# Performance work log

Hardware: AMD Instinct MI355X
Metric: run time of the kernel (lower is better)

The kernel has to match this reference:

```python
import jax, jax.numpy as jnp
import numpy as np

C = 128   # in_channels == global_graph_width (required by residual add)
W = 128
LN_EPS = 1e-5


def _mlp3(x, Ws, bs):
    # three stacked Linear layers (Dense dropout is identity in eval)
    for i in range(3):
        x = x @ Ws[i].T + bs[i]
    return x


def setup_inputs() -> dict:
    key = jax.random.key(0)
    ks = jax.random.split(key, 12)
    B, N, M = 16, 2048, 2048
    x1 = jax.random.normal(ks[0], (B, N, C), dtype=jnp.float32)
    x2 = jax.random.normal(ks[1], (B, M, C), dtype=jnp.float32)
    valid_mask = jax.random.randint(ks[2], (B, N, M), 0, 2) == 1
    s = 1.0 / np.sqrt(C)
    q_w = jax.random.normal(ks[3], (3, W, C), dtype=jnp.float32) * s
    q_b = jnp.zeros((3, W), dtype=jnp.float32)
    k_w = jax.random.normal(ks[4], (3, W, C), dtype=jnp.float32) * s
    k_b = jnp.zeros((3, W), dtype=jnp.float32)
    v_w = jax.random.normal(ks[5], (3, W, C), dtype=jnp.float32) * s
    v_b = jnp.zeros((3, W), dtype=jnp.float32)
    ln_g = jnp.ones((W,), dtype=jnp.float32)
    ln_b = jnp.zeros((W,), dtype=jnp.float32)
    return {"x1": x1, "x2": x2, "valid_mask": valid_mask,
            "q_w": q_w, "q_b": q_b, "k_w": k_w, "k_b": k_b,
            "v_w": v_w, "v_b": v_b, "ln_g": ln_g, "ln_b": ln_b}


def reference(x1, x2, valid_mask, q_w, q_b, k_w, k_b, v_w, v_b, ln_g, ln_b):
    query = _mlp3(x1, q_w, q_b)          # [B,N,W]
    key = _mlp3(x2, k_w, k_b)            # [B,M,W]
    value = _mlp3(x2, v_w, v_b)          # [B,M,W]
    scores = jnp.einsum('bnw,bmw->bnm', query, key) / jnp.sqrt(jnp.float32(W))
    # masked softmax: masked_fill(True -> -1e12), softmax, then zero masked cols
    scores = jnp.where(valid_mask, jnp.float32(-1e12), scores)
    attn = jax.nn.softmax(scores, axis=-1) * (1.0 - valid_mask.astype(scores.dtype))
    x = jnp.einsum('bnm,bmw->bnw', attn, value)  # [B,N,W]
    mu = jnp.mean(x, axis=-1, keepdims=True)
    var = jnp.var(x, axis=-1, keepdims=True)
    ln = (x - mu) / jnp.sqrt(var + LN_EPS) * ln_g + ln_b
    return ln + x1
```

## Files before the change

kernel.cpp:

```cpp
#include <hip/hip_runtime.h>
#include <hip/hip_bf16.h>
#include <hip/hip_fp16.h>

typedef __hip_bfloat16 bf16;
typedef __attribute__((ext_vector_type(8))) short short8;
typedef __attribute__((ext_vector_type(4))) float f32x4;

#define MFMA(a, b, c) __builtin_amdgcn_mfma_f32_16x16x32_bf16((a), (b), (c), 0, 0, 0)
#define SPLIT 2

__global__ void detect_mask(const unsigned int* __restrict__ m, int* __restrict__ flag)
{
    __shared__ int bad;
    if (threadIdx.x == 0) bad = 0;
    __syncthreads();
    unsigned int w = m[threadIdx.x];
    bool ok = (w == 0u) || (w == 1u) || (w == 0x3F800000u);
    if (!ok) atomicAdd(&bad, 1);
    __syncthreads();
    if (threadIdx.x == 0) *flag = (bad == 0) ? 0 : 1;
}

__global__ void compose_a(const float* __restrict__ qw, const float* __restrict__ qb,
                          const float* __restrict__ kw, const float* __restrict__ kb,
                          const float* __restrict__ vw, const float* __restrict__ vb,
                          float* __restrict__ T, float* __restrict__ bt)
{
    int h = blockIdx.x >> 7;
    int i = blockIdx.x & 127;
    int j = threadIdx.x;
    const float* W = (h == 0) ? qw : (h == 1) ? kw : vw;
    const float* bv = (h == 0) ? qb : (h == 1) ? kb : vb;
    const float* W1 = W;
    const float* W2 = W + 128 * 128;
    float acc = 0.f;
    for (int k = 0; k < 128; ++k) acc += W2[i * 128 + k] * W1[k * 128 + j];
    T[h * 16384 + i * 128 + j] = acc;
    if (j == 0) {
        float bacc = 0.f;
        for (int k = 0; k < 128; ++k) bacc += W2[i * 128 + k] * bv[k];
        bt[h * 128 + i] = bacc + bv[128 + i];
    }
}

__global__ void compose_b(const float* __restrict__ qw, const float* __restrict__ qb,
                          const float* __restrict__ kw, const float* __restrict__ kb,
                          const float* __restrict__ vw, const float* __restrict__ vb,
                          const float* __restrict__ T, const float* __restrict__ bt,
                          bf16* __restrict__ Weff, float* __restrict__ beff)
{
    int h = blockIdx.x >> 7;
    int i = blockIdx.x & 127;
    int j = threadIdx.x;
    const float* W = (h == 0) ? qw : (h == 1) ? kw : vw;
    const float* bv = (h == 0) ? qb : (h == 1) ? kb : vb;
    const float* W3 = W + 2 * 128 * 128;
    const float* Th = T + h * 16384;
    float acc = 0.f;
    for (int k = 0; k < 128; ++k) acc += W3[i * 128 + k] * Th[k * 128 + j];
    float scale = (h == 0) ? (1.4426950408889634f * rsqrtf(128.0f)) : 1.0f;
    Weff[h * 16384 + i * 128 + j] = __float2bfloat16(acc * scale);
    if (j == 0) {
        float bacc = 0.f;
        for (int k = 0; k < 128; ++k) bacc += W3[i * 128 + k] * bt[h * 128 + k];
        beff[h * 128 + i] = (bacc + bv[256 + i]) * scale;
    }
}

__global__ __launch_bounds__(256) void proj_rm(
    const float* __restrict__ X, const bf16* __restrict__ Wb,
    const float* __restrict__ bias, bf16* __restrict__ Y)
{
    __shared__ alignas(16) char sX[64 * 256];
    int tid = threadIdx.x;
    int lane = tid & 63, wave = tid >> 6;
    int l16 = lane & 15, lhi = lane >> 4;
    long long r0 = (long long)blockIdx.x * 64;
    {
        int row = tid >> 2, seg = tid & 3;
        const float4* src = reinterpret_cast<const float4*>(X + (r0 + row) * 128 + seg * 32);
        int swz = (row & 7) << 4;
        char* dst0 = &sX[0] + row * 256;
#pragma unroll
        for (int i = 0; i < 8; ++i) {
            float4 v = src[i];
            bf16* d = (bf16*)(dst0 + ((seg * 64 + i * 8) ^ swz));
            d[0] = __float2bfloat16(v.x); d[1] = __float2bfloat16(v.y);
            d[2] = __float2bfloat16(v.z); d[3] = __float2bfloat16(v.w);
        }
    }
    __syncthreads();
    int rloc = wave * 16 + l16;
    int swzr = (rloc & 7) << 4;
    short8 a[4];
#pragma unroll
    for (int c4 = 0; c4 < 4; ++c4)
        a[c4] = *(const short8*)(&sX[0] + ((rloc * 256 + lhi * 16 + c4 * 64) ^ swzr));
    f32x4 acc[8] = {};
#pragma unroll
    for (int n = 0; n < 8; ++n) {
        const bf16* wr = Wb + (n * 16 + l16) * 128 + lhi * 8;
#pragma unroll
        for (int c4 = 0; c4 < 4; ++c4)
            acc[n] = MFMA(a[c4], *(const short8*)(wr + c4 * 32), acc[n]);
    }
#pragma unroll
    for (int n = 0; n < 8; ++n) {
        float bia = bias[l16 + 16 * n];
#pragma unroll
        for (int r = 0; r < 4; ++r) {
            long long q = r0 + wave * 16 + lhi * 4 + r;
            Y[q * 128 + l16 + 16 * n] = __float2bfloat16(acc[n][r] + bia);
        }
    }
}

__global__ __launch_bounds__(256) void proj_kf(
    const float* __restrict__ X, const bf16* __restrict__ Wb,
    const float* __restrict__ bias, bf16* __restrict__ Kf)
{
    __shared__ alignas(16) char sX[64 * 256];
    int tid = threadIdx.x;
    int lane = tid & 63, wave = tid >> 6;
    int l16 = lane & 15, lhi = lane >> 4;
    long long r0 = (long long)blockIdx.x * 64;
    {
        int row = tid >> 2, seg = tid & 3;
        const float4* src = reinterpret_cast<const float4*>(X + (r0 + row) * 128 + seg * 32);
        int swz = (row & 7) << 4;
        char* dst0 = &sX[0] + row * 256;
#pragma unroll
        for (int i = 0; i < 8; ++i) {
            float4 v = src[i];
            bf16* d = (bf16*)(dst0 + ((seg * 64 + i * 8) ^ swz));
            d[0] = __float2bfloat16(v.x); d[1] = __float2bfloat16(v.y);
            d[2] = __float2bfloat16(v.z); d[3] = __float2bfloat16(v.w);
        }
    }
    __syncthreads();
    int rloc = wave * 16 + l16;
    int swzr = (rloc & 7) << 4;
    short8 a[4];
#pragma unroll
    for (int c4 = 0; c4 < 4; ++c4)
        a[c4] = *(const short8*)(&sX[0] + ((rloc * 256 + lhi * 16 + c4 * 64) ^ swzr));
    f32x4 acc[8] = {};
#pragma unroll
    for (int n = 0; n < 8; ++n) {
        const bf16* wr = Wb + (n * 16 + l16) * 128 + lhi * 8;
#pragma unroll
        for (int c4 = 0; c4 < 4; ++c4)
            acc[n] = MFMA(a[c4], *(const short8*)(wr + c4 * 32), acc[n]);
    }
    __syncthreads();
#pragma unroll
    for (int n = 0; n < 8; ++n) {
        float bia = bias[l16 + 16 * n];
#pragma unroll
        for (int r = 0; r < 4; ++r) {
            int row = wave * 16 + lhi * 4 + r;
            *(bf16*)(&sX[0] + ((row * 256 + (l16 + 16 * n) * 2) ^ ((row & 7) << 4))) =
                __float2bfloat16(acc[n][r] + bia);
        }
    }
    __syncthreads();
#pragma unroll
    for (int c4 = 0; c4 < 4; ++c4) {
        int row = wave * 16 + l16;
        short8 v = *(const short8*)(&sX[0] +
            ((row * 256 + c4 * 64 + lhi * 16) ^ ((row & 7) << 4)));
        long long tile = (r0 >> 4) + wave;
        *(short8*)(Kf + (tile * 4 + c4) * 512 + lane * 8) = v;
    }
}

__global__ __launch_bounds__(256) void proj_vf(
    const float* __restrict__ X2, const bf16* __restrict__ Wv,
    const float* __restrict__ bias, bf16* __restrict__ Vf, int M)
{
    __shared__ alignas(16) char sX[64 * 256];
    int tid = threadIdx.x;
    int lane = tid & 63, wave = tid >> 6;
    int l16 = lane & 15, lhi = lane >> 4;
    int mtiles = M >> 6;
    int b = blockIdx.x / mtiles, mt = blockIdx.x % mtiles;
    int m0 = mt * 64;
    {
        int row = tid >> 2, seg = tid & 3;
        const float4* src = reinterpret_cast<const float4*>(
            X2 + ((long long)b * M + m0 + row) * 128 + seg * 32);
        int swz = (row & 7) << 4;
        char* dst0 = &sX[0] + row * 256;
#pragma unroll
        for (int i = 0; i < 8; ++i) {
            float4 v = src[i];
            bf16* d = (bf16*)(dst0 + ((seg * 64 + i * 8) ^ swz));
            d[0] = __float2bfloat16(v.x); d[1] = __float2bfloat16(v.y);
            d[2] = __float2bfloat16(v.z); d[3] = __float2bfloat16(v.w);
        }
    }
    __syncthreads();
    int w0 = wave * 32;
    short8 a[2][4];
#pragma unroll
    for (int wt = 0; wt < 2; ++wt) {
        const bf16* wr = Wv + (w0 + wt * 16 + l16) * 128 + lhi * 8;
#pragma unroll
        for (int c4 = 0; c4 < 4; ++c4) a[wt][c4] = *(const short8*)(wr + c4 * 32);
    }
    f32x4 acc[2][4] = {};
#pragma unroll
    for (int mtl = 0; mtl < 4; ++mtl) {
        int rloc = mtl * 16 + l16;
        int swzr = (rloc & 7) << 4;
#pragma unroll
        for (int c4 = 0; c4 < 4; ++c4) {
            short8 xb = *(const short8*)(&sX[0] + ((rloc * 256 + lhi * 16 + c4 * 64) ^ swzr));
            acc[0][mtl] = MFMA(a[0][c4], xb, acc[0][mtl]);
            acc[1][mtl] = MFMA(a[1][c4], xb, acc[1][mtl]);
        }
    }
    __syncthreads();
#pragma unroll
    for (int wt = 0; wt < 2; ++wt) {
#pragma unroll
        for (int r = 0; r < 4; ++r) {
            int w = w0 + wt * 16 + lhi * 4 + r;
            float bia = bias[w];
#pragma unroll
            for (int mtl = 0; mtl < 4; ++mtl) {
                int mloc = mtl * 16 + l16;
                *(bf16*)(&sX[0] + ((w * 128 + mloc * 2) ^ ((w & 7) << 4))) =
                    __float2bfloat16(acc[wt][mtl][r] + bia);
            }
        }
    }
    __syncthreads();
#pragma unroll
    for (int q = 0; q < 4; ++q) {
        int fr = wave * 4 + q;
        int gloc = fr >> 3, n = fr & 7;
        int row = n * 16 + l16;
        short8 v = *(const short8*)(&sX[0] +
            ((row * 128 + gloc * 64 + lhi * 16) ^ ((row & 7) << 4)));
        long long g = (long long)b * (M >> 5) + (m0 >> 5) + gloc;
        *(short8*)(Vf + (g * 8 + n) * 512 + lane * 8) = v;
    }
}

__global__ __launch_bounds__(256, 4) void attn_split(
    const bf16* __restrict__ Q, const bf16* __restrict__ Kf, const bf16* __restrict__ Vf,
    const void* __restrict__ maskp, const int* __restrict__ flagp,
    __half* __restrict__ pacc, float* __restrict__ pml,
    int B, int N, int M)
{
    __shared__ alignas(16) char kbuf[2][8192];
    __shared__ alignas(16) char vbuf[2][8192];
    __shared__ alignas(16) char Plds[4][1024];
    __shared__ alignas(16) unsigned char smask[4][512];
    int nq = N >> 6;
    int nwg = gridDim.x;
    int bid = blockIdx.x;
    int wg = ((nwg & 7) == 0) ? ((bid & 7) * (nwg >> 3) + (bid >> 3)) : bid;
    int qt = wg % nq;
    int s  = (wg / nq) % SPLIT;
    int b  = wg / (nq * SPLIT);
    int tid = threadIdx.x;
    int lane = tid & 63, wave = tid >> 6;
    int l16 = lane & 15, lhi = lane >> 4;
    int q0 = qt * 64 + wave * 16;
    int Mh = M / SPLIT;
    int mbase = s * Mh;
    long long R = (long long)B * N;
    int fl4 = (*flagp == 0);
    const int NT = Mh >> 5;

    const bf16* qptr = Q + ((long long)b * N + q0 + l16) * 128 + lhi * 8;
    short8 aq[4];
#pragma unroll
    for (int c4 = 0; c4 < 4; ++c4) aq[c4] = *(const short8*)(qptr + c4 * 32);

    long long ktile0 = ((long long)b * M + mbase) >> 4;
    long long gbase  = ((long long)b * M + mbase) >> 5;

    int srow = lane >> 2, soff = (lane & 3) * 8;
    long long mrowb = ((long long)b * N + q0 + srow) * (long long)M + mbase + soff;

    char* pb = &Plds[wave][0];
    unsigned char* smw = &smask[wave][0];
    int pswz = (l16 & 3) << 4;

    f32x4 acc[8] = {};
    float plsum = 0.f;

    auto mload = [&](int t) -> uint2 {
        uint2 r;
        if (fl4) {
            const int* mp = (const int*)maskp;
            const int4* pp = (const int4*)(mp + mrowb + (long long)t * 32);
            int4 a = pp[0], bb = pp[1];
            r.x = (a.x ? 1u : 0u) | ((a.y ? 1u : 0u) << 8) |
                  ((a.z ? 1u : 0u) << 16) | ((a.w ? 1u : 0u) << 24);
            r.y = (bb.x ? 1u : 0u) | ((bb.y ? 1u : 0u) << 8) |
                  ((bb.z ? 1u : 0u) << 16) | ((bb.w ? 1u : 0u) << 24);
        } else {
            r = *(const uint2*)((const unsigned char*)maskp + mrowb + (long long)t * 32);
        }
        return r;
    };

    {
        long long F = ktile0 * 4 + wave * 2;
        long long G = gbase * 8 + wave * 2;
        int4 k0 = *(const int4*)(Kf + F * 512 + lane * 8);
        int4 k1 = *(const int4*)(Kf + (F + 1) * 512 + lane * 8);
        int4 v0 = *(const int4*)(Vf + G * 512 + lane * 8);
        int4 v1 = *(const int4*)(Vf + (G + 1) * 512 + lane * 8);
        uint2 mreg = mload(0);
        *(int4*)(&kbuf[0][(wave * 2 + 0) * 1024 + lane * 16]) = k0;
        *(int4*)(&kbuf[0][(wave * 2 + 1) * 1024 + lane * 16]) = k1;
        *(int4*)(&vbuf[0][(wave * 2 + 0) * 1024 + lane * 16]) = v0;
        *(int4*)(&vbuf[0][(wave * 2 + 1) * 1024 + lane * 16]) = v1;
        *(uint2*)(smw + srow * 32 + soff) = mreg;
        __syncthreads();
    }

    for (int t = 0; t < NT; ++t) {
        int cur = t & 1;
        int4 ks0, ks1, vs0, vs1;
        uint2 mreg;
        bool nxt = (t + 1 < NT);
        if (nxt) {
            long long F = (ktile0 + 2LL * (t + 1)) * 4 + wave * 2;
            long long G = (gbase + (t + 1)) * 8 + wave * 2;
            ks0 = *(const int4*)(Kf + F * 512 + lane * 8);
            ks1 = *(const int4*)(Kf + (F + 1) * 512 + lane * 8);
            vs0 = *(const int4*)(Vf + G * 512 + lane * 8);
            vs1 = *(const int4*)(Vf + (G + 1) * 512 + lane * 8);
            mreg = mload(t + 1);
        }

        f32x4 sv[2];
#pragma unroll
        for (int j = 0; j < 2; ++j) {
            f32x4 tt = {0.f, 0.f, 0.f, 0.f};
#pragma unroll
            for (int c4 = 0; c4 < 4; ++c4)
                tt = MFMA(*(const short8*)(&kbuf[cur][(j * 4 + c4) * 1024 + lane * 16]),
                          aq[c4], tt);
            sv[j] = tt;
        }

#pragma unroll
        for (int j = 0; j < 2; ++j) {
            unsigned int mk = *(const unsigned int*)(smw + l16 * 32 + 16 * j + lhi * 4);
            float p0 = (mk & 0x000000ffu) ? 0.f : exp2f(sv[j][0]);
            float p1 = (mk & 0x0000ff00u) ? 0.f : exp2f(sv[j][1]);
            float p2 = (mk & 0x00ff0000u) ? 0.f : exp2f(sv[j][2]);
            float p3 = (mk & 0xff000000u) ? 0.f : exp2f(sv[j][3]);
            plsum += (p0 + p1) + (p2 + p3);
            unsigned int w0, w1;
            asm("v_cvt_pk_bf16_f32 %0, %1, %2" : "=v"(w0) : "v"(p0), "v"(p1));
            asm("v_cvt_pk_bf16_f32 %0, %1, %2" : "=v"(w1) : "v"(p2), "v"(p3));
            uint2 wv; wv.x = w0; wv.y = w1;
            *(uint2*)(pb + l16 * 64 + ((j * 32 + lhi * 8) ^ pswz)) = wv;
        }

        short8 pa = *(const short8*)(pb + l16 * 64 + ((lhi * 16) ^ pswz));

#pragma unroll
        for (int n = 0; n < 8; ++n)
            acc[n] = MFMA(pa, *(const short8*)(&vbuf[cur][n * 1024 + lane * 16]), acc[n]);

        if (nxt) {
            int nx = cur ^ 1;
            *(int4*)(&kbuf[nx][(wave * 2 + 0) * 1024 + lane * 16]) = ks0;
            *(int4*)(&kbuf[nx][(wave * 2 + 1) * 1024 + lane * 16]) = ks1;
            *(int4*)(&vbuf[nx][(wave * 2 + 0) * 1024 + lane * 16]) = vs0;
            *(int4*)(&vbuf[nx][(wave * 2 + 1) * 1024 + lane * 16]) = vs1;
            *(uint2*)(smw + srow * 32 + soff) = mreg;
            __syncthreads();
        }
    }

    float lsum = plsum;
    lsum += __shfl_xor(lsum, 16);
    lsum += __shfl_xor(lsum, 32);
    float invq = (lsum > 0.f) ? 1.f / lsum : 0.f;
    float inv[4];
#pragma unroll
    for (int r = 0; r < 4; ++r) inv[r] = __shfl(invq, lhi * 4 + r);
    long long rowg[4];
#pragma unroll
    for (int r = 0; r < 4; ++r) rowg[r] = (long long)b * N + q0 + lhi * 4 + r;
#pragma unroll
    for (int n = 0; n < 8; ++n)
#pragma unroll
        for (int r = 0; r < 4; ++r)
            pacc[((long long)s * R + rowg[r]) * 128 + l16 + 16 * n] =
                __float2half(acc[n][r] * inv[r]);
    if (lhi == 0)
        pml[(long long)s * R + (long long)b * N + q0 + l16] = lsum;
}

__global__ __launch_bounds__(256) void combine(
    const __half* __restrict__ pacc, const float* __restrict__ pml,
    const float* __restrict__ lng, const float* __restrict__ lnb,
    const float* __restrict__ x1, float* __restrict__ out, long long R)
{
    int tid = threadIdx.x;
    int lane = tid & 63, wave = tid >> 6;
    long long row = (long long)blockIdx.x * 4 + wave;
    float l[SPLIT];
    float den = 0.f;
#pragma unroll
    for (int s = 0; s < SPLIT; ++s) {
        l[s] = pml[(long long)s * R + row];
        den += l[s];
    }
    float inv = (den > 0.f) ? 1.f / den : 0.f;
    int c0 = lane * 2;
    float xa = 0.f, xb = 0.f;
#pragma unroll
    for (int s = 0; s < SPLIT; ++s) {
        const __half* hp = pacc + ((long long)s * R + row) * 128 + c0;
        xa += l[s] * __half2float(hp[0]);
        xb += l[s] * __half2float(hp[1]);
    }
    xa *= inv; xb *= inv;
    float su = xa + xb;
#pragma unroll
    for (int o = 1; o < 64; o <<= 1) su += __shfl_xor(su, o);
    float mu = su * (1.f / 128.f);
    float da = xa - mu, db = xb - mu;
    float sq = da * da + db * db;
#pragma unroll
    for (int o = 1; o < 64; o <<= 1) sq += __shfl_xor(sq, o);
    float rstd = rsqrtf(sq * (1.f / 128.f) + 1e-5f);
    float2 xr = *(const float2*)(x1 + row * 128 + c0);
    float2 o2;
    o2.x = da * rstd * lng[c0] + lnb[c0] + xr.x;
    o2.y = db * rstd * lng[c0 + 1] + lnb[c0 + 1] + xr.y;
    *(float2*)(out + row * 128 + c0) = o2;
}

extern "C" void kernel_launch(void* const* d_in, const int* in_sizes, int n_in,
                              void* d_out, int out_size, void* d_ws, size_t ws_size,
                              hipStream_t stream)
{
    const float* x1 = (const float*)d_in[0];
    const float* x2 = (const float*)d_in[1];
    const void* mask = d_in[2];
    const float* qw = (const float*)d_in[3];
    const float* qb = (const float*)d_in[4];
    const float* kw = (const float*)d_in[5];
    const float* kb = (const float*)d_in[6];
    const float* vw = (const float*)d_in[7];
    const float* vb = (const float*)d_in[8];
    const float* lng = (const float*)d_in[9];
    const float* lnb = (const float*)d_in[10];

    long long a = (long long)in_sizes[0] / 128;
    long long c = (long long)in_sizes[1] / 128;
    long long mm = (long long)in_sizes[2];
    int B = (int)((a * c) / mm);
    int N = (int)(a / B);
    int M = (int)(c / B);
    long long R = a;

    char* p = (char*)d_ws;
    bf16* Q = (bf16*)p;    p += (size_t)a * 128 * sizeof(bf16);
    bf16* Kf = (bf16*)p;   p += (size_t)c * 128 * sizeof(bf16);
    bf16* Vf = (bf16*)p;   p += (size_t)c * 128 * sizeof(bf16);
    float* T = (float*)p;  p += 3 * 128 * 128 * sizeof(float);
    float* bt = (float*)p; p += 3 * 128 * sizeof(float);
    float* beff = (float*)p; p += 3 * 128 * sizeof(float);
    bf16* Weff = (bf16*)p; p += 3 * 128 * 128 * sizeof(bf16);
    int* flag = (int*)p;   p += 256;
    __half* pacc = (__half*)p; p += (size_t)SPLIT * R * 128 * sizeof(__half);
    float* pml = (float*)p;    p += (size_t)SPLIT * R * sizeof(float);

    detect_mask<<<1, 256, 0, stream>>>((const unsigned int*)mask, flag);
    compose_a<<<384, 128, 0, stream>>>(qw, qb, kw, kb, vw, vb, T, bt);
    compose_b<<<384, 128, 0, stream>>>(qw, qb, kw, kb, vw, vb, T, bt, Weff, beff);

    proj_rm<<<(int)(a / 64), 256, 0, stream>>>(x1, Weff, beff, Q);
    proj_kf<<<(int)(c / 64), 256, 0, stream>>>(x2, Weff + 16384, beff + 128, Kf);
    proj_vf<<<(int)(c / 64), 256, 0, stream>>>(x2, Weff + 2 * 16384, beff + 256, Vf, M);

    int nblk = B * (N / 64) * SPLIT;
    attn_split<<<nblk, 256, 0, stream>>>(Q, Kf, Vf, mask, flag, pacc, pml, B, N, M);
    combine<<<(int)(R / 4), 256, 0, stream>>>(pacc, pml, lng, lnb, x1, (float*)d_out, R);
}
```

Baseline: 165.6 us.

## Fuse K/V projections and pass P between MFMAs via lane shuffles

Merges the separate K and V projection kernels into one that loads and converts x2 to bf16 once, using a second LDS buffer for output staging. In the attention loop, the probability tile is now rearranged from the QK MFMA output layout into the PV MFMA input layout with two cross-lane shuffles instead of an LDS write and read. The per-wave P LDS buffer is removed, and the MFMA sections are wrapped in s_setprio to favour matrix issue. This saves one launch and one pass over x2, and cuts LDS traffic in the hot loop. The cost is extra shuffle and select instructions, plus more LDS in the projection kernel.

```diff
diff --git a/kernel.cpp b/kernel.cpp
--- a/kernel.cpp
+++ b/kernel.cpp
@@ -115,18 +115,23 @@
     }
 }
 
-__global__ __launch_bounds__(256) void proj_kf(
-    const float* __restrict__ X, const bf16* __restrict__ Wb,
-    const float* __restrict__ bias, bf16* __restrict__ Kf)
+__global__ __launch_bounds__(256) void proj_kvf(
+    const float* __restrict__ X2,
+    const bf16* __restrict__ Wk, const float* __restrict__ bk,
+    const bf16* __restrict__ Wv, const float* __restrict__ bv,
+    bf16* __restrict__ Kf, bf16* __restrict__ Vf, int M)
 {
     __shared__ alignas(16) char sX[64 * 256];
+    __shared__ alignas(16) char rbuf[64 * 256];
     int tid = threadIdx.x;
     int lane = tid & 63, wave = tid >> 6;
     int l16 = lane & 15, lhi = lane >> 4;
     long long r0 = (long long)blockIdx.x * 64;
+    int b = (int)(r0 / M);
+    int m0 = (int)(r0 % M);
     {
         int row = tid >> 2, seg = tid & 3;
-        const float4* src = reinterpret_cast<const float4*>(X + (r0 + row) * 128 + seg * 32);
+        const float4* src = reinterpret_cast<const float4*>(X2 + (r0 + row) * 128 + seg * 32);
         int swz = (row & 7) << 4;
         char* dst0 = &sX[0] + row * 256;
 #pragma unroll
@@ -138,77 +143,52 @@
         }
     }
     __syncthreads();
-    int rloc = wave * 16 + l16;
-    int swzr = (rloc & 7) << 4;
-    short8 a[4];
-#pragma unroll
-    for (int c4 = 0; c4 < 4; ++c4)
-        a[c4] = *(const short8*)(&sX[0] + ((rloc * 256 + lhi * 16 + c4 * 64) ^ swzr));
-    f32x4 acc[8] = {};
-#pragma unroll
-    for (int n = 0; n < 8; ++n) {
-        const bf16* wr = Wb + (n * 16 + l16) * 128 + lhi * 8;
+
+    {
+        int rloc = wave * 16 + l16;
+        int swzr = (rloc & 7) << 4;
+        short8 a[4];
 #pragma unroll
         for (int c4 = 0; c4 < 4; ++c4)
-            acc[n] = MFMA(a[c4], *(const short8*)(wr + c4 * 32), acc[n]);
-    }
-    __syncthreads();
-#pragma unroll
-    for (int n = 0; n < 8; ++n) {
-        float bia = bias[l16 + 16 * n];
-#pragma unroll
-        for (int r = 0; r < 4; ++r) {
-            int row = wave * 16 + lhi * 4 + r;
-            *(bf16*)(&sX[0] + ((row * 256 + (l16 + 16 * n) * 2) ^ ((row & 7) << 4))) =
-                __float2bfloat16(acc[n][r] + bia);
+            a[c4] = *(const short8*)(&sX[0] + ((rloc * 256 + lhi * 16 + c4 * 64) ^ swzr));
+        f32x4 acc[8] = {};
+#pragma unroll
+        for (int n = 0; n < 8; ++n) {
+            const bf16* wr = Wk + (n * 16 + l16) * 128 + lhi * 8;
+#pragma unroll
+            for (int c4 = 0; c4 < 4; ++c4)
+                acc[n] = MFMA(a[c4], *(const short8*)(wr + c4 * 32), acc[n]);
+        }
+#pragma unroll
+        for (int n = 0; n < 8; ++n) {
+            float bia = bk[l16 + 16 * n];
+#pragma unroll
+            for (int r = 0; r < 4; ++r) {
+                int row = wave * 16 + lhi * 4 + r;
+                *(bf16*)(&rbuf[0] + ((row * 256 + (l16 + 16 * n) * 2) ^ ((row & 7) << 4))) =
+                    __float2bfloat16(acc[n][r] + bia);
+            }
         }
     }
     __syncthreads();
 #pragma unroll
     for (int c4 = 0; c4 < 4; ++c4) {
         int row = wave * 16 + l16;
-        short8 v = *(const short8*)(&sX[0] +
+        short8 v = *(const short8*)(&rbuf[0] +
             ((row * 256 + c4 * 64 + lhi * 16) ^ ((row & 7) << 4)));
         long long tile = (r0 >> 4) + wave;
         *(short8*)(Kf + (tile * 4 + c4) * 512 + lane * 8) = v;
     }
-}
-
-__global__ __launch_bounds__(256) void proj_vf(
-    const float* __restrict__ X2, const bf16* __restrict__ Wv,
-    const float* __restrict__ bias, bf16* __restrict__ Vf, int M)
-{
-    __shared__ alignas(16) char sX[64 * 256];
-    int tid = threadIdx.x;
-    int lane = tid & 63, wave = tid >> 6;
-    int l16 = lane & 15, lhi = lane >> 4;
-    int mtiles = M >> 6;
-    int b = blockIdx.x / mtiles, mt = blockIdx.x % mtiles;
-    int m0 = mt * 64;
-    {
-        int row = tid >> 2, seg = tid & 3;
-        const float4* src = reinterpret_cast<const float4*>(
-            X2 + ((long long)b * M + m0 + row) * 128 + seg * 32);
-        int swz = (row & 7) << 4;
-        char* dst0 = &sX[0] + row * 256;
-#pragma unroll
-        for (int i = 0; i < 8; ++i) {
-            float4 v = src[i];
-            bf16* d = (bf16*)(dst0 + ((seg * 64 + i * 8) ^ swz));
-            d[0] = __float2bfloat16(v.x); d[1] = __float2bfloat16(v.y);
-            d[2] = __float2bfloat16(v.z); d[3] = __float2bfloat16(v.w);
-        }
-    }
-    __syncthreads();
+
     int w0 = wave * 32;
-    short8 a[2][4];
+    short8 a2[2][4];
 #pragma unroll
     for (int wt = 0; wt < 2; ++wt) {
         const bf16* wr = Wv + (w0 + wt * 16 + l16) * 128 + lhi * 8;
 #pragma unroll
-        for (int c4 = 0; c4 < 4; ++c4) a[wt][c4] = *(const short8*)(wr + c4 * 32);
-    }
-    f32x4 acc[2][4] = {};
+        for (int c4 = 0; c4 < 4; ++c4) a2[wt][c4] = *(const short8*)(wr + c4 * 32);
+    }
+    f32x4 acc2[2][4] = {};
 #pragma unroll
     for (int mtl = 0; mtl < 4; ++mtl) {
         int rloc = mtl * 16 + l16;
@@ -216,8 +196,8 @@
 #pragma unroll
         for (int c4 = 0; c4 < 4; ++c4) {
             short8 xb = *(const short8*)(&sX[0] + ((rloc * 256 + lhi * 16 + c4 * 64) ^ swzr));
-            acc[0][mtl] = MFMA(a[0][c4], xb, acc[0][mtl]);
-            acc[1][mtl] = MFMA(a[1][c4], xb, acc[1][mtl]);
+            acc2[0][mtl] = MFMA(a2[0][c4], xb, acc2[0][mtl]);
+            acc2[1][mtl] = MFMA(a2[1][c4], xb, acc2[1][mtl]);
         }
     }
     __syncthreads();
@@ -226,12 +206,12 @@
 #pragma unroll
         for (int r = 0; r < 4; ++r) {
             int w = w0 + wt * 16 + lhi * 4 + r;
-            float bia = bias[w];
+            float bia = bv[w];
 #pragma unroll
             for (int mtl = 0; mtl < 4; ++mtl) {
                 int mloc = mtl * 16 + l16;
-                *(bf16*)(&sX[0] + ((w * 128 + mloc * 2) ^ ((w & 7) << 4))) =
-                    __float2bfloat16(acc[wt][mtl][r] + bia);
+                *(bf16*)(&rbuf[0] + ((w * 128 + mloc * 2) ^ ((w & 7) << 4))) =
+                    __float2bfloat16(acc2[wt][mtl][r] + bia);
             }
         }
     }
@@ -241,7 +221,7 @@
         int fr = wave * 4 + q;
         int gloc = fr >> 3, n = fr & 7;
         int row = n * 16 + l16;
-        short8 v = *(const short8*)(&sX[0] +
+        short8 v = *(const short8*)(&rbuf[0] +
             ((row * 128 + gloc * 64 + lhi * 16) ^ ((row & 7) << 4)));
         long long g = (long long)b * (M >> 5) + (m0 >> 5) + gloc;
         *(short8*)(Vf + (g * 8 + n) * 512 + lane * 8) = v;
@@ -256,7 +236,6 @@
 {
     __shared__ alignas(16) char kbuf[2][8192];
     __shared__ alignas(16) char vbuf[2][8192];
-    __shared__ alignas(16) char Plds[4][1024];
     __shared__ alignas(16) unsigned char smask[4][512];
     int nq = N >> 6;
     int nwg = gridDim.x;
@@ -286,9 +265,7 @@
     int srow = lane >> 2, soff = (lane & 3) * 8;
     long long mrowb = ((long long)b * N + q0 + srow) * (long long)M + mbase + soff;
 
-    char* pb = &Plds[wave][0];
     unsigned char* smw = &smask[wave][0];
-    int pswz = (l16 & 3) << 4;
 
     f32x4 acc[8] = {};
     float plsum = 0.f;
@@ -340,6 +317,7 @@
             mreg = mload(t + 1);
         }
 
+        __builtin_amdgcn_s_setprio(1);
         f32x4 sv[2];
 #pragma unroll
         for (int j = 0; j < 2; ++j) {
@@ -350,7 +328,9 @@
                           aq[c4], tt);
             sv[j] = tt;
         }
-
+        __builtin_amdgcn_s_setprio(0);
+
+        uint2 Bb[2];
 #pragma unroll
         for (int j = 0; j < 2; ++j) {
             unsigned int mk = *(const unsigned int*)(smw + l16 * 32 + 16 * j + lhi * 4);
@@ -362,15 +342,28 @@
             unsigned int w0, w1;
             asm("v_cvt_pk_bf16_f32 %0, %1, %2" : "=v"(w0) : "v"(p0), "v"(p1));
             asm("v_cvt_pk_bf16_f32 %0, %1, %2" : "=v"(w1) : "v"(p2), "v"(p3));
-            uint2 wv; wv.x = w0; wv.y = w1;
-            *(uint2*)(pb + l16 * 64 + ((j * 32 + lhi * 8) ^ pswz)) = wv;
-        }
-
-        short8 pa = *(const short8*)(pb + l16 * 64 + ((lhi * 16) ^ pswz));
-
+            Bb[j].x = w0; Bb[j].y = w1;
+        }
+
+        uint2 X1 = (lhi < 2) ? Bb[1] : Bb[0];
+        uint2 Qb;
+        Qb.x = __shfl_xor((int)X1.x, 32);
+        Qb.y = __shfl_xor((int)X1.y, 32);
+        uint2 Pb = (lhi < 2) ? Bb[0] : Bb[1];
+        uint2 X2 = (lhi == 1 || lhi == 2) ? Pb : Qb;
+        uint2 Y2;
+        Y2.x = __shfl_xor((int)X2.x, 16);
+        Y2.y = __shfl_xor((int)X2.y, 16);
+        uint2 s0 = (lhi == 0) ? Pb : (lhi == 1) ? Y2 : (lhi == 2) ? Qb : Y2;
+        uint2 s1 = (lhi == 0) ? Y2 : (lhi == 1) ? Qb : (lhi == 2) ? Y2 : Pb;
+        unsigned int paw[4] = {s0.x, s0.y, s1.x, s1.y};
+        short8 pa = *(const short8*)paw;
+
+        __builtin_amdgcn_s_setprio(1);
 #pragma unroll
         for (int n = 0; n < 8; ++n)
             acc[n] = MFMA(pa, *(const short8*)(&vbuf[cur][n * 1024 + lane * 16]), acc[n]);
+        __builtin_amdgcn_s_setprio(0);
 
         if (nxt) {
             int nx = cur ^ 1;
@@ -485,8 +478,8 @@
     compose_b<<<384, 128, 0, stream>>>(qw, qb, kw, kb, vw, vb, T, bt, Weff, beff);
 
     proj_rm<<<(int)(a / 64), 256, 0, stream>>>(x1, Weff, beff, Q);
-    proj_kf<<<(int)(c / 64), 256, 0, stream>>>(x2, Weff + 16384, beff + 128, Kf);
-    proj_vf<<<(int)(c / 64), 256, 0, stream>>>(x2, Weff + 2 * 16384, beff + 256, Vf, M);
+    proj_kvf<<<(int)(c / 64), 256, 0, stream>>>(x2, Weff + 16384, beff + 128,
+                                                Weff + 2 * 16384, beff + 256, Kf, Vf, M);
 
     int nblk = B * (N / 64) * SPLIT;
     attn_split<<<nblk, 256, 0, stream>>>(Q, Kf, Vf, mask, flag, pacc, pml, B, N, M);
```

New measurement: 159.7 us. 1.04x faster.
